# Kernel optimization log

Measured on AMD Instinct MI355X. Metric: run time of the kernel, lower is better.

Reference implementation:

```python
import jax, jax.numpy as jnp
import numpy as np

EMBED = 1024
HEADS = 16
DEPTH = EMBED // HEADS
FFN_DIM = 4096
EPS = 1e-9


def layer_norm(x, g, b):
    mu = jnp.mean(x, axis=-1, keepdims=True)
    var = jnp.mean(jnp.square(x - mu), axis=-1, keepdims=True)
    return (x - mu) * jax.lax.rsqrt(var + EPS) * g + b


def setup_inputs() -> dict:
    key = jax.random.key(0)
    ks = jax.random.split(key, 16)
    B, S = 2, 2048
    s_e = 1.0 / np.sqrt(EMBED)
    s_f = 1.0 / np.sqrt(FFN_DIM)
    return {
        "x": jax.random.normal(ks[0], (B, S, EMBED), dtype=jnp.float32),
        "mask": jnp.zeros((B, 1, 1, S), dtype=jnp.float32),
        "wq_w": jax.random.normal(ks[1], (EMBED, EMBED), dtype=jnp.float32) * s_e,
        "wq_b": jnp.zeros((EMBED,), dtype=jnp.float32),
        "wk_w": jax.random.normal(ks[2], (EMBED, EMBED), dtype=jnp.float32) * s_e,
        "wk_b": jnp.zeros((EMBED,), dtype=jnp.float32),
        "wv_w": jax.random.normal(ks[3], (EMBED, EMBED), dtype=jnp.float32) * s_e,
        "wv_b": jnp.zeros((EMBED,), dtype=jnp.float32),
        "wo_w": jax.random.normal(ks[4], (EMBED, EMBED), dtype=jnp.float32) * s_e,
        "wo_b": jnp.zeros((EMBED,), dtype=jnp.float32),
        "f1_w": jax.random.normal(ks[5], (EMBED, FFN_DIM), dtype=jnp.float32) * s_e,
        "f1_b": jnp.zeros((FFN_DIM,), dtype=jnp.float32),
        "f2_w": jax.random.normal(ks[6], (FFN_DIM, EMBED), dtype=jnp.float32) * s_f,
        "f2_b": jnp.zeros((EMBED,), dtype=jnp.float32),
        "ln1_g": jnp.ones((EMBED,), dtype=jnp.float32),
        "ln1_b": jnp.zeros((EMBED,), dtype=jnp.float32),
        "ln2_g": jnp.ones((EMBED,), dtype=jnp.float32),
        "ln2_b": jnp.zeros((EMBED,), dtype=jnp.float32),
    }


def reference(x, mask, wq_w, wq_b, wk_w, wk_b, wv_w, wv_b, wo_w, wo_b,
              f1_w, f1_b, f2_w, f2_b, ln1_g, ln1_b, ln2_g, ln2_b):
    B, S, E = x.shape

    def split_heads(t):  # (B,S,E) -> (B,H,S,D)
        return t.reshape(B, S, HEADS, DEPTH).transpose(0, 2, 1, 3)

    q = split_heads(x @ wq_w + wq_b)
    k = split_heads(x @ wk_w + wk_b)
    v = split_heads(x @ wv_w + wv_b)

    logits = jnp.einsum("bhqd,bhkd->bhqk", q, k) / jnp.sqrt(jnp.float32(DEPTH))
    logits = logits + mask * -1e12  # mask broadcast (B,1,1,S)
    attn = jax.nn.softmax(logits, axis=-1)
    out = jnp.einsum("bhqk,bhkd->bhqd", attn, v)
    out = out.transpose(0, 2, 1, 3).reshape(B, S, E)
    out = out @ wo_w + wo_b

    # dropout is identity (is_train=False)
    h = layer_norm(out + x, ln1_g, ln1_b)
    f = jax.nn.relu(h @ f1_w + f1_b) @ f2_w + f2_b
    return layer_norm(f + h, ln2_g, ln2_b)
```

## Files before the change

### kernel.cpp

```cpp
#include <hip/hip_runtime.h>
#include <hip/hip_bf16.h>
#include <stdint.h>

typedef __hip_bfloat16 bf16;
typedef __attribute__((ext_vector_type(8))) short short8;
typedef __attribute__((ext_vector_type(4))) short short4v;
typedef __attribute__((ext_vector_type(4))) float floatx4;

#define E_DIM 1024
#define S_LEN 2048
#define NB    2
#define NH    16
#define HD    64
#define FFN   4096
#define MTOT  4096

#define QSCALE 0.18033688011112042f
#define MSCALE -1.4426950408889634e12f

__device__ __forceinline__ void gl_lds16(const void* g, void* l) {
  __builtin_amdgcn_global_load_lds(
      (__attribute__((address_space(1))) void*)(g),
      (__attribute__((address_space(3))) void*)(l), 16, 0, 0);
}

#define VMW(N)  do { asm volatile("s_waitcnt vmcnt(" #N ")" ::: "memory"); \
                     __builtin_amdgcn_sched_barrier(0); } while (0)
#define LGKM0   do { asm volatile("s_waitcnt lgkmcnt(0)" ::: "memory"); } while (0)
#define BARR    do { asm volatile("s_barrier" ::: "memory"); } while (0)

__device__ __forceinline__ float exp2_fast(float x) {
  float r;
  asm("v_exp_f32 %0, %1" : "=v"(r) : "v"(x));
  return r;
}

__device__ __forceinline__ int fswz_v(int row) { return row & 7; }
__device__ __forceinline__ int fswz_k(int row) {
  return ((row ^ (row >> 3)) & 3) | ((((row >> 3) ^ (row >> 4)) & 1) << 2);
}

__device__ __forceinline__ float bf16bits2float(short s) {
  union { unsigned u; float f; } c;
  c.u = ((unsigned)(unsigned short)s) << 16;
  return c.f;
}

__global__ __launch_bounds__(256)
void cvt_bf16(const float* __restrict__ in, bf16* __restrict__ out) {
  const size_t i = ((size_t)blockIdx.x * 256 + threadIdx.x) * 4;
  float4 v = *(const float4*)(in + i);
  out[i + 0] = __float2bfloat16(v.x);
  out[i + 1] = __float2bfloat16(v.y);
  out[i + 2] = __float2bfloat16(v.z);
  out[i + 3] = __float2bfloat16(v.w);
}

__global__ __launch_bounds__(256)
void transpose_all(const float* __restrict__ wq, const float* __restrict__ wk,
                   const float* __restrict__ wv, const float* __restrict__ wo,
                   const float* __restrict__ f1, const float* __restrict__ f2,
                   bf16* __restrict__ W3T, bf16* __restrict__ woT,
                   bf16* __restrict__ f1T, bf16* __restrict__ f2T) {
  const int z = blockIdx.z;
  const float* in;
  bf16* out;
  int inStride, outStride, rOff, cOff;
  if (z < 4) {
    in = (z == 0) ? wq : (z == 1) ? wk : (z == 2) ? wv : wo;
    out = (z < 3) ? (W3T + (size_t)z * 1024 * 1024) : woT;
    inStride = 1024; outStride = 1024; rOff = 0; cOff = 0;
  } else if (z < 8) {
    in = f1; out = f1T; inStride = 4096; outStride = 1024;
    rOff = 0; cOff = (z - 4) * 1024;
  } else {
    in = f2; out = f2T; inStride = 1024; outStride = 4096;
    rOff = (z - 8) * 1024; cOff = 0;
  }
  __shared__ float tile[32][33];
  const int tx = threadIdx.x & 31;
  const int ty = threadIdx.x >> 5;
  const int c0 = blockIdx.x * 32;
  const int r0 = blockIdx.y * 32;
#pragma unroll
  for (int j = 0; j < 32; j += 8)
    tile[ty + j][tx] =
        in[(size_t)(rOff + r0 + ty + j) * inStride + cOff + c0 + tx];
  __syncthreads();
#pragma unroll
  for (int j = 0; j < 32; j += 8)
    out[(size_t)(cOff + c0 + ty + j) * outStride + rOff + r0 + tx] =
        __float2bfloat16(tile[tx][ty + j]);
}

__global__ __launch_bounds__(256)
void prep_bias(const float* __restrict__ qb, const float* __restrict__ kb,
               const float* __restrict__ vb, float* __restrict__ out) {
  const int i = blockIdx.x * 256 + threadIdx.x;
  float v = (i < 1024) ? qb[i] * QSCALE
                       : ((i < 2048) ? kb[i - 1024] : vb[i - 2048]);
  out[i] = v;
}

__global__ __launch_bounds__(512, 2)
void gemm256(const bf16* __restrict__ A, const bf16* __restrict__ B,
             const float* __restrict__ bias, void* __restrict__ Cout,
             void* __restrict__ Cout2,
             int M, int N, int Kpart, int lda, int mode) {
  __shared__ alignas(16) bf16 sA[2][2][128 * 64];
  __shared__ alignas(16) bf16 sB[2][2][128 * 64];
  const int tid   = threadIdx.x;
  const int wave  = tid >> 6;
  const int lane  = tid & 63;
  const int row16 = lane & 15;
  const int quad  = lane >> 4;
  const int sw7   = row16 & 7;

  const int gx = gridDim.x;
  const int nwg = gx * gridDim.y;
  const int cpx = nwg >> 3;
  int id = blockIdx.y * gx + blockIdx.x;
  id = (id & 7) * cpx + (id >> 3);
  const int m0 = (id % gx) * 256;
  const int n0 = (id / gx) * 256;

  const int wm2 = wave >> 2;
  const int wn4 = wave & 3;
  const int wm  = wm2 * 128;
  const int wn  = wn4 * 64;
  const int hB  = wn4 >> 1;
  const int rbB = (wn4 & 1) * 64;
  const int koff = blockIdx.z * Kpart;
  const int NS = Kpart >> 6;

  floatx4 acc[8][4];
#pragma unroll
  for (int i = 0; i < 8; i++)
#pragma unroll
    for (int j = 0; j < 4; j++) {
      floatx4 z = {0.f, 0.f, 0.f, 0.f};
      acc[i][j] = z;
    }

  auto stage_half = [&](const bf16* G, int rowBase, int k0, bf16* dst) {
#pragma unroll
    for (int j = 0; j < 2; ++j) {
      const int r = wave * 16 + j * 8 + (lane >> 3);
      const int g = (lane & 7) ^ (r & 7);
      gl_lds16(G + (size_t)(rowBase + r) * lda + k0 + g * 8,
               dst + (wave * 16 + j * 8) * 64);
    }
  };
  auto stage_tile = [&](int t, int p) {
    const int k0 = koff + t * 64;
    stage_half(A, m0,       k0, &sA[p][0][0]);
    stage_half(A, m0 + 128, k0, &sA[p][1][0]);
    stage_half(B, n0,       k0, &sB[p][0][0]);
    stage_half(B, n0 + 128, k0, &sB[p][1][0]);
  };

  short8 aF[8][2];
  short8 bF[4][2];
  const bf16* aH = nullptr;
  const bf16* bH = nullptr;

  auto read_aF = [&](int mi0) {
#pragma unroll
    for (int mi = 0; mi < 4; ++mi)
#pragma unroll
      for (int kk = 0; kk < 2; ++kk)
        aF[mi0 + mi][kk] = *(const short8*)(
            aH + ((mi0 + mi) * 16 + row16) * 64 + (((kk * 4 + quad) ^ sw7) << 3));
  };
  auto read_bF = [&](int ni0) {
#pragma unroll
    for (int ni = 0; ni < 2; ++ni)
#pragma unroll
      for (int kk = 0; kk < 2; ++kk)
        bF[ni0 + ni][kk] = *(const short8*)(
            bH + (rbB + (ni0 + ni) * 16 + row16) * 64 + (((kk * 4 + quad) ^ sw7) << 3));
  };
  auto qmf = [&](int mi0, int ni0) {
    __builtin_amdgcn_s_setprio(1);
#pragma unroll
    for (int mi = 0; mi < 4; ++mi)
#pragma unroll
      for (int ni = 0; ni < 2; ++ni)
#pragma unroll
        for (int kk = 0; kk < 2; ++kk)
          acc[mi0 + mi][ni0 + ni] = __builtin_amdgcn_mfma_f32_16x16x32_bf16(
              aF[mi0 + mi][kk], bF[ni0 + ni][kk], acc[mi0 + mi][ni0 + ni], 0, 0, 0);
    __builtin_amdgcn_s_setprio(0);
  };

  stage_tile(0, 0);
  stage_tile(1, 1);

  for (int s = 0; s < NS; ++s) {
    const int b = s & 1;
    aH = &sA[b][wm2][0];
    bH = &sB[b][hB][0];
    if (s + 1 < NS) VMW(8); else VMW(0);
    BARR;
    read_bF(0);
    read_bF(2);
    read_aF(0);
    qmf(0, 0);
    qmf(0, 2);
    read_aF(4);
    LGKM0;
    BARR;
    if (s + 2 < NS) stage_tile(s + 2, b);
    qmf(4, 0);
    qmf(4, 2);
  }

  float bval[4] = {0.f, 0.f, 0.f, 0.f};
  if (mode != 0) {
#pragma unroll
    for (int ni = 0; ni < 4; ni++) bval[ni] = bias[n0 + wn + ni * 16 + row16];
  }

#pragma unroll
  for (int mi = 0; mi < 8; mi++) {
#pragma unroll
    for (int ni = 0; ni < 4; ni++) {
      const int col = n0 + wn + ni * 16 + row16;
      if (mode == 0) {
        float* co = (float*)((blockIdx.z < 2) ? Cout : Cout2) +
                    (size_t)(blockIdx.z & 1) * M * N;
#pragma unroll
        for (int r = 0; r < 4; r++) {
          const int row = m0 + wm + mi * 16 + quad * 4 + r;
          co[(size_t)row * N + col] = acc[mi][ni][r];
        }
      } else if (mode == 1) {
#pragma unroll
        for (int r = 0; r < 4; r++) {
          const int row = m0 + wm + mi * 16 + quad * 4 + r;
          float v = acc[mi][ni][r] + bval[ni];
          v = v > 0.f ? v : 0.f;
          ((bf16*)Cout)[(size_t)row * N + col] = __float2bfloat16(v);
        }
      } else {
        const int mat = col >> 10;
        const int c10 = col & 1023;
        const int hh = c10 >> 6, dd = c10 & 63;
        const float scl = (mat == 0) ? QSCALE : 1.0f;
        bf16* qout = (bf16*)Cout;
        const int rbase = m0 + wm + mi * 16 + quad * 4;
        const int b2 = rbase >> 11, ss = rbase & 2047;
        const size_t bh = (size_t)b2 * NH + hh;
        if (mat == 2) {
          bf16* vt = qout + (1 << 23);
          short4v pv;
#pragma unroll
          for (int r = 0; r < 4; r++) {
            bf16 t = __float2bfloat16(acc[mi][ni][r] + bval[ni]);
            pv[r] = *(short*)&t;
          }
          *(short4v*)(vt + (bh * HD + dd) * S_LEN + ss) = pv;
        } else {
          bf16* o = (mat == 1) ? (qout + (1 << 22)) : qout;
#pragma unroll
          for (int r = 0; r < 4; r++) {
            float v = acc[mi][ni][r] * scl + bval[ni];
            o[(bh * S_LEN + ss + r) * HD + dd] = __float2bfloat16(v);
          }
        }
      }
    }
  }
}

__global__ __launch_bounds__(256, 2)
void flash_attn(const bf16* __restrict__ Q, const bf16* __restrict__ K,
                const bf16* __restrict__ Vt, const float* __restrict__ mask,
                bf16* __restrict__ Out) {
  __shared__ alignas(16) bf16 sK[2][64 * 64];
  __shared__ alignas(16) bf16 sV[2][64 * 64];
  __shared__ alignas(16) float sM[S_LEN];

  const int tid   = threadIdx.x;
  const int wave  = tid >> 6;
  const int lane  = tid & 63;
  const int row16 = lane & 15;
  const int quad  = lane >> 4;
  const int bh = blockIdx.y;
  const int b = bh >> 4, h = bh & 15;
  const int q0 = blockIdx.x * 128;
  const int qg = q0 + wave * 32 + row16;

  const bf16* qpA = Q + ((size_t)bh * S_LEN + qg) * HD;
  const bf16* qpB = qpA + 16 * HD;
  short8 qa0 = *(const short8*)(qpA + quad * 8);
  short8 qa1 = *(const short8*)(qpA + 32 + quad * 8);
  short8 qb0 = *(const short8*)(qpB + quad * 8);
  short8 qb1 = *(const short8*)(qpB + 32 + quad * 8);

  for (int i = tid; i < S_LEN / 4; i += 256) {
    float4 mv = ((const float4*)(mask + (size_t)b * S_LEN))[i];
    float4 w = {MSCALE * mv.x, MSCALE * mv.y, MSCALE * mv.z, MSCALE * mv.w};
    ((float4*)sM)[i] = w;
  }
  LGKM0;

  short8 ones;
#pragma unroll
  for (int j = 0; j < 8; j++) ones[j] = (short)0x3F80;

  floatx4 laccA = {0.f, 0.f, 0.f, 0.f};
  floatx4 laccB = {0.f, 0.f, 0.f, 0.f};
  floatx4 ovA[4], ovB[4];
#pragma unroll
  for (int i = 0; i < 4; i++) {
    floatx4 z = {0.f,0.f,0.f,0.f};
    ovA[i] = z; ovB[i] = z;
  }

  const bf16* Kbase = K + (size_t)bh * S_LEN * HD;
  const bf16* Vbase = Vt + (size_t)bh * HD * S_LEN;
  const int NT = S_LEN / 64;

  auto stage = [&](int kt) {
    const bf16* Kg = Kbase + (size_t)kt * 64 * HD;
    const bf16* Vg = Vbase + kt * 64;
    bf16* dK = sK[kt & 1];
    bf16* dV = sV[kt & 1];
#pragma unroll
    for (int j = 0; j < 2; ++j) {
      const int ch = wave * 2 + j;
      const int row = ch * 8 + (lane >> 3);
      const int sc_ = lane & 7;
      gl_lds16(Kg + row * 64 + ((sc_ ^ fswz_k(row)) * 8), dK + ch * 512);
      gl_lds16(Vg + (size_t)row * S_LEN + ((sc_ ^ fswz_v(row)) * 8), dV + ch * 512);
    }
  };

  stage(0);

  for (int kt = 0; kt < NT; ++kt) {
    if (kt + 1 < NT) {
      stage(kt + 1);
      VMW(4);
    } else {
      VMW(0);
    }
    BARR;

    const bf16* Kb = sK[kt & 1];
    const bf16* Vb = sV[kt & 1];

    floatx4 scA[4], scB[4];
#pragma unroll
    for (int mi = 0; mi < 4; mi++) {
      const int row = ((row16 >> 2) << 3) + (row16 & 3) + ((mi & 1) << 2) + ((mi >> 1) << 5);
      const int fk = fswz_k(row);
      short8 kf0 = *(const short8*)(Kb + row * 64 + ((quad ^ fk) << 3));
      short8 kf1 = *(const short8*)(Kb + row * 64 + (((4 + quad) ^ fk) << 3));
      floatx4 zA = {0.f, 0.f, 0.f, 0.f};
      zA = __builtin_amdgcn_mfma_f32_16x16x32_bf16(kf0, qa0, zA, 0, 0, 0);
      scA[mi] = __builtin_amdgcn_mfma_f32_16x16x32_bf16(kf1, qa1, zA, 0, 0, 0);
      floatx4 zB = {0.f, 0.f, 0.f, 0.f};
      zB = __builtin_amdgcn_mfma_f32_16x16x32_bf16(kf0, qb0, zB, 0, 0, 0);
      scB[mi] = __builtin_amdgcn_mfma_f32_16x16x32_bf16(kf1, qb1, zB, 0, 0, 0);
    }

#pragma unroll
    for (int mi = 0; mi < 4; mi++) {
      float4 mv = *(const float4*)(sM + kt * 64 + (quad << 3) + ((mi & 1) << 2) + ((mi >> 1) << 5));
      scA[mi][0] = exp2_fast(scA[mi][0] + mv.x);
      scA[mi][1] = exp2_fast(scA[mi][1] + mv.y);
      scA[mi][2] = exp2_fast(scA[mi][2] + mv.z);
      scA[mi][3] = exp2_fast(scA[mi][3] + mv.w);
      scB[mi][0] = exp2_fast(scB[mi][0] + mv.x);
      scB[mi][1] = exp2_fast(scB[mi][1] + mv.y);
      scB[mi][2] = exp2_fast(scB[mi][2] + mv.z);
      scB[mi][3] = exp2_fast(scB[mi][3] + mv.w);
    }

    short8 pfA[2], pfB[2];
#pragma unroll
    for (int ks = 0; ks < 2; ks++)
#pragma unroll
      for (int jp = 0; jp < 4; jp++) {
        const int mi = 2 * ks + (jp >> 1);
        const int r0 = (jp & 1) * 2;
        bf16 a0 = __float2bfloat16(scA[mi][r0]);
        bf16 a1 = __float2bfloat16(scA[mi][r0 + 1]);
        pfA[ks][2 * jp]     = *(short*)&a0;
        pfA[ks][2 * jp + 1] = *(short*)&a1;
        bf16 b0 = __float2bfloat16(scB[mi][r0]);
        bf16 b1 = __float2bfloat16(scB[mi][r0 + 1]);
        pfB[ks][2 * jp]     = *(short*)&b0;
        pfB[ks][2 * jp + 1] = *(short*)&b1;
      }

    laccA = __builtin_amdgcn_mfma_f32_16x16x32_bf16(ones, pfA[0], laccA, 0, 0, 0);
    laccA = __builtin_amdgcn_mfma_f32_16x16x32_bf16(ones, pfA[1], laccA, 0, 0, 0);
    laccB = __builtin_amdgcn_mfma_f32_16x16x32_bf16(ones, pfB[0], laccB, 0, 0, 0);
    laccB = __builtin_amdgcn_mfma_f32_16x16x32_bf16(ones, pfB[1], laccB, 0, 0, 0);

#pragma unroll
    for (int mi = 0; mi < 4; mi++) {
      const int row = mi * 16 + row16;
      const int fv = fswz_v(row);
      short8 v0 = *(const short8*)(Vb + row * 64 + ((quad ^ fv) << 3));
      short8 v1 = *(const short8*)(Vb + row * 64 + (((4 + quad) ^ fv) << 3));
      ovA[mi] = __builtin_amdgcn_mfma_f32_16x16x32_bf16(v0, pfA[0], ovA[mi], 0, 0, 0);
      ovA[mi] = __builtin_amdgcn_mfma_f32_16x16x32_bf16(v1, pfA[1], ovA[mi], 0, 0, 0);
      ovB[mi] = __builtin_amdgcn_mfma_f32_16x16x32_bf16(v0, pfB[0], ovB[mi], 0, 0, 0);
      ovB[mi] = __builtin_amdgcn_mfma_f32_16x16x32_bf16(v1, pfB[1], ovB[mi], 0, 0, 0);
    }
    BARR;
  }

  const float invA = 1.0f / laccA[0];
  const float invB = 1.0f / laccB[0];
#pragma unroll
  for (int mi = 0; mi < 4; mi++) {
    short4v pva, pvb;
#pragma unroll
    for (int r = 0; r < 4; r++) {
      bf16 ta = __float2bfloat16(ovA[mi][r] * invA);
      pva[r] = *(short*)&ta;
      bf16 tb = __float2bfloat16(ovB[mi][r] * invB);
      pvb[r] = *(short*)&tb;
    }
    *(short4v*)(Out + ((size_t)(b * S_LEN + qg)) * E_DIM + h * HD + mi * 16 + quad * 4) = pva;
    *(short4v*)(Out + ((size_t)(b * S_LEN + qg + 16)) * E_DIM + h * HD + mi * 16 + quad * 4) = pvb;
  }
}

__global__ __launch_bounds__(256)
void ln_reduce(const float* __restrict__ p0, const float* __restrict__ p1,
               const float* __restrict__ p2, const float* __restrict__ p3,
               const float* __restrict__ resf, const bf16* __restrict__ resb,
               const float* __restrict__ bias, const float* __restrict__ g,
               const float* __restrict__ be, float* __restrict__ outf,
               bf16* __restrict__ outb) {
  const int row = blockIdx.x;
  const int tid = threadIdx.x;
  const size_t base = (size_t)row * 1024;
  const int c = tid * 4;
  float4 a = *(const float4*)(p0 + base + c);
  float4 bq = *(const float4*)(p1 + base + c);
  float4 xv;
  xv.x = a.x + bq.x;
  xv.y = a.y + bq.y;
  xv.z = a.z + bq.z;
  xv.w = a.w + bq.w;
  if (p2) {
    float4 a2 = *(const float4*)(p2 + base + c);
    float4 a3 = *(const float4*)(p3 + base + c);
    xv.x += a2.x + a3.x;
    xv.y += a2.y + a3.y;
    xv.z += a2.z + a3.z;
    xv.w += a2.w + a3.w;
  }
  float4 rv;
  if (resf) {
    rv = *(const float4*)(resf + base + c);
  } else {
    short4v rb = *(const short4v*)((const short*)resb + base + c);
    rv.x = bf16bits2float(rb[0]);
    rv.y = bf16bits2float(rb[1]);
    rv.z = bf16bits2float(rb[2]);
    rv.w = bf16bits2float(rb[3]);
  }
  float4 bi = *(const float4*)(bias + c);
  xv.x += rv.x + bi.x;
  xv.y += rv.y + bi.y;
  xv.z += rv.z + bi.z;
  xv.w += rv.w + bi.w;
  float s  = xv.x + xv.y + xv.z + xv.w;
  float s2 = xv.x * xv.x + xv.y * xv.y + xv.z * xv.z + xv.w * xv.w;
#pragma unroll
  for (int d = 1; d < 64; d <<= 1) {
    s  += __shfl_xor(s, d);
    s2 += __shfl_xor(s2, d);
  }
  __shared__ float red[2][4];
  const int wave = tid >> 6;
  if ((tid & 63) == 0) { red[0][wave] = s; red[1][wave] = s2; }
  __syncthreads();
  s  = red[0][0] + red[0][1] + red[0][2] + red[0][3];
  s2 = red[1][0] + red[1][1] + red[1][2] + red[1][3];
  const float mu  = s * (1.0f / 1024.0f);
  const float var = s2 * (1.0f / 1024.0f) - mu * mu;
  const float rs  = rsqrtf(var + 1e-9f);
  float4 gg = *(const float4*)(g + c);
  float4 bb = *(const float4*)(be + c);
  float4 y;
  y.x = (xv.x - mu) * rs * gg.x + bb.x;
  y.y = (xv.y - mu) * rs * gg.y + bb.y;
  y.z = (xv.z - mu) * rs * gg.z + bb.z;
  y.w = (xv.w - mu) * rs * gg.w + bb.w;
  if (outf) *(float4*)(outf + base + c) = y;
  if (outb) {
    bf16* o = outb + base + c;
    o[0] = __float2bfloat16(y.x);
    o[1] = __float2bfloat16(y.y);
    o[2] = __float2bfloat16(y.z);
    o[3] = __float2bfloat16(y.w);
  }
}

extern "C" void kernel_launch(void* const* d_in, const int* in_sizes, int n_in,
                              void* d_out, int out_size, void* d_ws,
                              size_t ws_size, hipStream_t stream) {
  const float* x    = (const float*)d_in[0];
  const float* mask = (const float*)d_in[1];
  const float* wq_w = (const float*)d_in[2];
  const float* wq_b = (const float*)d_in[3];
  const float* wk_w = (const float*)d_in[4];
  const float* wk_b = (const float*)d_in[5];
  const float* wv_w = (const float*)d_in[6];
  const float* wv_b = (const float*)d_in[7];
  const float* wo_w = (const float*)d_in[8];
  const float* wo_b = (const float*)d_in[9];
  const float* f1_w = (const float*)d_in[10];
  const float* f1_b = (const float*)d_in[11];
  const float* f2_w = (const float*)d_in[12];
  const float* f2_b = (const float*)d_in[13];
  const float* ln1_g = (const float*)d_in[14];
  const float* ln1_b = (const float*)d_in[15];
  const float* ln2_g = (const float*)d_in[16];
  const float* ln2_b = (const float*)d_in[17];
  float* out = (float*)d_out;

  char* ws = (char*)d_ws;
  const size_t MB = 1u << 20;
  bf16*  xbf   = (bf16*)(ws + 0 * MB);
  bf16*  W3T   = (bf16*)(ws + 8 * MB);
  bf16*  woT   = (bf16*)(ws + 14 * MB);
  float* bqkv  = (float*)(ws + 16 * MB);
  bf16*  Qb    = (bf16*)(ws + 17 * MB);
  bf16*  attnb = (bf16*)(ws + 0 * MB);
  bf16*  ffn1  = (bf16*)(ws + 17 * MB);
  bf16*  f1T   = (bf16*)(ws + 49 * MB);
  bf16*  f2T   = (bf16*)(ws + 57 * MB);
  float* P01   = (float*)(ws + 65 * MB);
  bf16*  hbf   = (bf16*)(ws + 97 * MB);
  float* P23   = (float*)(ws + 105 * MB);
  const size_t PS = (size_t)MTOT * E_DIM;

  const int KS = (ws_size >= (size_t)137 * MB) ? 4 : 2;
  const float* p2 = (KS == 4) ? P23 : nullptr;
  const float* p3 = (KS == 4) ? P23 + PS : nullptr;

  cvt_bf16<<<4096, 256, 0, stream>>>(x, xbf);
  transpose_all<<<dim3(32, 32, 12), 256, 0, stream>>>(
      wq_w, wk_w, wv_w, wo_w, f1_w, f2_w, W3T, woT, f1T, f2T);
  prep_bias<<<12, 256, 0, stream>>>(wq_b, wk_b, wv_b, bqkv);

  gemm256<<<dim3(16, 12, 1), 512, 0, stream>>>(
      xbf, W3T, bqkv, Qb, nullptr, MTOT, 3 * E_DIM, E_DIM, E_DIM, 2);

  flash_attn<<<dim3(S_LEN / 128, NB * NH), 256, 0, stream>>>(
      Qb, Qb + (1 << 22), Qb + (1 << 23), mask, attnb);

  gemm256<<<dim3(16, 4, KS), 512, 0, stream>>>(
      attnb, woT, nullptr, P01, P23, MTOT, E_DIM, E_DIM / KS, E_DIM, 0);

  ln_reduce<<<MTOT, 256, 0, stream>>>(P01, P01 + PS, p2, p3, x, nullptr,
                                      wo_b, ln1_g, ln1_b, nullptr, hbf);

  gemm256<<<dim3(16, 16, 1), 512, 0, stream>>>(
      hbf, f1T, f1_b, ffn1, nullptr, MTOT, FFN, E_DIM, E_DIM, 1);

  gemm256<<<dim3(16, 4, KS), 512, 0, stream>>>(
      ffn1, f2T, nullptr, P01, P23, MTOT, E_DIM, FFN / KS, FFN, 0);

  ln_reduce<<<MTOT, 256, 0, stream>>>(P01, P01 + PS, p2, p3, nullptr, hbf,
                                      f2_b, ln2_g, ln2_b, out, nullptr);
}
```

Before: 356.0 us.

## Replace 256x256 GEMM tiles with 128x128 tiles and K-step 32

Swaps the 512-thread 256x256-tile GEMM for a 256-thread 128x128-tile kernel with 32-wide K steps, a smaller LDS footprint and three blocks per CU. The swizzle and fragment loading are redone for 32-column LDS rows. The intent is more workgroups per GEMM and better occupancy and CU fill for these problem sizes. In exchange, each tile reuses data less, so global and LDS traffic per FLOP rises and barriers happen twice as often per unit of K.

After: 381.1 us. 7.1% more time.

```diff
diff --git a/kernel.cpp b/kernel.cpp
--- a/kernel.cpp
+++ b/kernel.cpp
@@ -102,94 +102,73 @@
   out[i] = v;
 }
 
-__global__ __launch_bounds__(512, 2)
-void gemm256(const bf16* __restrict__ A, const bf16* __restrict__ B,
+__global__ __launch_bounds__(256, 3)
+void gemm128(const bf16* __restrict__ A, const bf16* __restrict__ B,
              const float* __restrict__ bias, void* __restrict__ Cout,
              void* __restrict__ Cout2,
              int M, int N, int Kpart, int lda, int mode) {
-  __shared__ alignas(16) bf16 sA[2][2][128 * 64];
-  __shared__ alignas(16) bf16 sB[2][2][128 * 64];
+  __shared__ alignas(16) bf16 sA[2][128 * 32];
+  __shared__ alignas(16) bf16 sB[2][128 * 32];
   const int tid   = threadIdx.x;
   const int wave  = tid >> 6;
   const int lane  = tid & 63;
   const int row16 = lane & 15;
   const int quad  = lane >> 4;
-  const int sw7   = row16 & 7;
+  const int sw3   = row16 & 3;
 
   const int gx = gridDim.x;
   const int nwg = gx * gridDim.y;
   const int cpx = nwg >> 3;
   int id = blockIdx.y * gx + blockIdx.x;
   id = (id & 7) * cpx + (id >> 3);
-  const int m0 = (id % gx) * 256;
-  const int n0 = (id / gx) * 256;
-
-  const int wm2 = wave >> 2;
-  const int wn4 = wave & 3;
-  const int wm  = wm2 * 128;
-  const int wn  = wn4 * 64;
-  const int hB  = wn4 >> 1;
-  const int rbB = (wn4 & 1) * 64;
+  const int m0 = (id % gx) * 128;
+  const int n0 = (id / gx) * 128;
+
+  const int wm = (wave >> 1) * 64;
+  const int wn = (wave & 1) * 64;
   const int koff = blockIdx.z * Kpart;
-  const int NS = Kpart >> 6;
-
-  floatx4 acc[8][4];
-#pragma unroll
-  for (int i = 0; i < 8; i++)
+  const int NS = Kpart >> 5;
+
+  floatx4 acc[4][4];
+#pragma unroll
+  for (int i = 0; i < 4; i++)
 #pragma unroll
     for (int j = 0; j < 4; j++) {
       floatx4 z = {0.f, 0.f, 0.f, 0.f};
       acc[i][j] = z;
     }
 
-  auto stage_half = [&](const bf16* G, int rowBase, int k0, bf16* dst) {
+  auto stage_tile = [&](int t, int p) {
+    const int k0 = koff + t * 32;
 #pragma unroll
     for (int j = 0; j < 2; ++j) {
-      const int r = wave * 16 + j * 8 + (lane >> 3);
-      const int g = (lane & 7) ^ (r & 7);
-      gl_lds16(G + (size_t)(rowBase + r) * lda + k0 + g * 8,
-               dst + (wave * 16 + j * 8) * 64);
+      const int r = j * 64 + wave * 16 + (lane >> 2);
+      const int g = (lane & 3) ^ (r & 3);
+      gl_lds16(A + (size_t)(m0 + r) * lda + k0 + g * 8,
+               sA[p] + (j * 64 + wave * 16) * 32);
+      gl_lds16(B + (size_t)(n0 + r) * lda + k0 + g * 8,
+               sB[p] + (j * 64 + wave * 16) * 32);
     }
   };
-  auto stage_tile = [&](int t, int p) {
-    const int k0 = koff + t * 64;
-    stage_half(A, m0,       k0, &sA[p][0][0]);
-    stage_half(A, m0 + 128, k0, &sA[p][1][0]);
-    stage_half(B, n0,       k0, &sB[p][0][0]);
-    stage_half(B, n0 + 128, k0, &sB[p][1][0]);
+
+  short8 aF[4], bF[4];
+  auto read_frags = [&](int p) {
+#pragma unroll
+    for (int i = 0; i < 4; ++i) {
+      const int ra = wm + i * 16 + row16;
+      const int rb = wn + i * 16 + row16;
+      aF[i] = *(const short8*)(sA[p] + ra * 32 + ((quad ^ sw3) << 3));
+      bF[i] = *(const short8*)(sB[p] + rb * 32 + ((quad ^ sw3) << 3));
+    }
   };
-
-  short8 aF[8][2];
-  short8 bF[4][2];
-  const bf16* aH = nullptr;
-  const bf16* bH = nullptr;
-
-  auto read_aF = [&](int mi0) {
+  auto qmf = [&](int ni0) {
+    __builtin_amdgcn_s_setprio(1);
 #pragma unroll
     for (int mi = 0; mi < 4; ++mi)
 #pragma unroll
-      for (int kk = 0; kk < 2; ++kk)
-        aF[mi0 + mi][kk] = *(const short8*)(
-            aH + ((mi0 + mi) * 16 + row16) * 64 + (((kk * 4 + quad) ^ sw7) << 3));
-  };
-  auto read_bF = [&](int ni0) {
-#pragma unroll
-    for (int ni = 0; ni < 2; ++ni)
-#pragma unroll
-      for (int kk = 0; kk < 2; ++kk)
-        bF[ni0 + ni][kk] = *(const short8*)(
-            bH + (rbB + (ni0 + ni) * 16 + row16) * 64 + (((kk * 4 + quad) ^ sw7) << 3));
-  };
-  auto qmf = [&](int mi0, int ni0) {
-    __builtin_amdgcn_s_setprio(1);
-#pragma unroll
-    for (int mi = 0; mi < 4; ++mi)
-#pragma unroll
       for (int ni = 0; ni < 2; ++ni)
-#pragma unroll
-        for (int kk = 0; kk < 2; ++kk)
-          acc[mi0 + mi][ni0 + ni] = __builtin_amdgcn_mfma_f32_16x16x32_bf16(
-              aF[mi0 + mi][kk], bF[ni0 + ni][kk], acc[mi0 + mi][ni0 + ni], 0, 0, 0);
+        acc[mi][ni0 + ni] = __builtin_amdgcn_mfma_f32_16x16x32_bf16(
+            aF[mi], bF[ni0 + ni], acc[mi][ni0 + ni], 0, 0, 0);
     __builtin_amdgcn_s_setprio(0);
   };
 
@@ -197,22 +176,15 @@
   stage_tile(1, 1);
 
   for (int s = 0; s < NS; ++s) {
-    const int b = s & 1;
-    aH = &sA[b][wm2][0];
-    bH = &sB[b][hB][0];
-    if (s + 1 < NS) VMW(8); else VMW(0);
+    const int p = s & 1;
+    if (s + 1 < NS) VMW(4); else VMW(0);
     BARR;
-    read_bF(0);
-    read_bF(2);
-    read_aF(0);
-    qmf(0, 0);
-    qmf(0, 2);
-    read_aF(4);
+    read_frags(p);
+    qmf(0);
     LGKM0;
     BARR;
-    if (s + 2 < NS) stage_tile(s + 2, b);
-    qmf(4, 0);
-    qmf(4, 2);
+    if (s + 2 < NS) stage_tile(s + 2, p);
+    qmf(2);
   }
 
   float bval[4] = {0.f, 0.f, 0.f, 0.f};
@@ -222,7 +194,7 @@
   }
 
 #pragma unroll
-  for (int mi = 0; mi < 8; mi++) {
+  for (int mi = 0; mi < 4; mi++) {
 #pragma unroll
     for (int ni = 0; ni < 4; ni++) {
       const int col = n0 + wn + ni * 16 + row16;
@@ -554,22 +526,22 @@
       wq_w, wk_w, wv_w, wo_w, f1_w, f2_w, W3T, woT, f1T, f2T);
   prep_bias<<<12, 256, 0, stream>>>(wq_b, wk_b, wv_b, bqkv);
 
-  gemm256<<<dim3(16, 12, 1), 512, 0, stream>>>(
+  gemm128<<<dim3(32, 24, 1), 256, 0, stream>>>(
       xbf, W3T, bqkv, Qb, nullptr, MTOT, 3 * E_DIM, E_DIM, E_DIM, 2);
 
   flash_attn<<<dim3(S_LEN / 128, NB * NH), 256, 0, stream>>>(
       Qb, Qb + (1 << 22), Qb + (1 << 23), mask, attnb);
 
-  gemm256<<<dim3(16, 4, KS), 512, 0, stream>>>(
+  gemm128<<<dim3(32, 8, KS), 256, 0, stream>>>(
       attnb, woT, nullptr, P01, P23, MTOT, E_DIM, E_DIM / KS, E_DIM, 0);
 
   ln_reduce<<<MTOT, 256, 0, stream>>>(P01, P01 + PS, p2, p3, x, nullptr,
                                       wo_b, ln1_g, ln1_b, nullptr, hbf);
 
-  gemm256<<<dim3(16, 16, 1), 512, 0, stream>>>(
+  gemm128<<<dim3(32, 32, 1), 256, 0, stream>>>(
       hbf, f1T, f1_b, ffn1, nullptr, MTOT, FFN, E_DIM, E_DIM, 1);
 
-  gemm256<<<dim3(16, 4, KS), 512, 0, stream>>>(
+  gemm128<<<dim3(32, 8, KS), 256, 0, stream>>>(
       ffn1, f2T, nullptr, P01, P23, MTOT, E_DIM, FFN / KS, FFN, 0);
 
   ln_reduce<<<MTOT, 256, 0, stream>>>(P01, P01 + PS, p2, p3, nullptr, hbf,
```
